# Kernel tuning notes

Measured on AMD Instinct MI355X. Metric: run time of the kernel, lower is better.

Reference implementation:

```python
import jax, jax.numpy as jnp
import numpy as np

NUM_LAYERS = 2
FEATURES = 128
INPUT_SIZE = 128
HIDDEN = 512
BATCH = 128
SEQ_LEN = 512
PRED_LEN = 128


def _uniform(key, shape, fan):
    bound = 1.0 / np.sqrt(fan)
    return jax.random.uniform(key, shape, jnp.float32, -bound, bound)


def setup_inputs() -> dict:
    key = jax.random.key(0)
    ks = jax.random.split(key, 14)
    inp = {}
    inp["x"] = jax.random.normal(ks[0], (BATCH, SEQ_LEN, FEATURES), jnp.float32)
    # encoder Linear(features -> input_size)
    inp["enc_w"] = _uniform(ks[1], (INPUT_SIZE, FEATURES), FEATURES)
    inp["enc_b"] = _uniform(ks[2], (INPUT_SIZE,), FEATURES)
    # decoder Linear(hidden -> input_size)
    inp["dec_w"] = _uniform(ks[3], (INPUT_SIZE, HIDDEN), HIDDEN)
    inp["dec_b"] = _uniform(ks[4], (INPUT_SIZE,), HIDDEN)
    # LSTM layer 0 (input_size -> hidden), gate order i,f,g,o as in PyTorch
    inp["wih0"] = _uniform(ks[5], (4 * HIDDEN, INPUT_SIZE), HIDDEN)
    inp["whh0"] = _uniform(ks[6], (4 * HIDDEN, HIDDEN), HIDDEN)
    inp["bih0"] = _uniform(ks[7], (4 * HIDDEN,), HIDDEN)
    inp["bhh0"] = _uniform(ks[8], (4 * HIDDEN,), HIDDEN)
    # LSTM layer 1 (hidden -> hidden)
    inp["wih1"] = _uniform(ks[9], (4 * HIDDEN, HIDDEN), HIDDEN)
    inp["whh1"] = _uniform(ks[10], (4 * HIDDEN, HIDDEN), HIDDEN)
    inp["bih1"] = _uniform(ks[11], (4 * HIDDEN,), HIDDEN)
    inp["bhh1"] = _uniform(ks[12], (4 * HIDDEN,), HIDDEN)
    inp["pred_len"] = PRED_LEN
    return inp


def _lstm_cell(h, c, inp, wih, whh, bih, bhh):
    g = inp @ wih.T + bih + h @ whh.T + bhh  # [B, 4H]
    i, f, gg, o = jnp.split(g, 4, axis=-1)
    c = jax.nn.sigmoid(f) * c + jax.nn.sigmoid(i) * jnp.tanh(gg)
    h = jax.nn.sigmoid(o) * jnp.tanh(c)
    return h, c


def reference(x, enc_w, enc_b, dec_w, dec_b, wih0, whh0, bih0, bhh0,
              wih1, whh1, bih1, bhh1, pred_len):
    B, S, Fdim = x.shape
    T = S + pred_len - 1
    # pad x to T steps; beyond S the input comes from the previous output
    x_pad = jnp.concatenate([x, jnp.zeros((B, pred_len - 1, Fdim), x.dtype)], axis=1)
    x_t = jnp.transpose(x_pad, (1, 0, 2))  # [T, B, F]

    def step(carry, xs):
        h0, c0, h1, c1, prev_out = carry
        xt, t = xs
        inp = jnp.where(t < S, xt, prev_out)
        e = inp @ enc_w.T + enc_b                    # encoder
        h0, c0 = _lstm_cell(h0, c0, e, wih0, whh0, bih0, bhh0)
        h1, c1 = _lstm_cell(h1, c1, h0, wih1, whh1, bih1, bhh1)
        out = h1 @ dec_w.T + dec_b                   # decoder
        return (h0, c0, h1, c1, out), out

    z = jnp.zeros((B, HIDDEN), x.dtype)
    init = (z, z, z, z, jnp.zeros((B, Fdim), x.dtype))
    _, outs = jax.lax.scan(step, init, (x_t, jnp.arange(T)))
    # keep steps idx >= S-1 (pred_len outputs), back to [B, pred_len, input_size]
    return jnp.transpose(outs[S - 1:], (1, 0, 2))
```

## Files before the change

### kernel.cpp

```cpp
#include <hip/hip_runtime.h>
#include <math.h>

#define HID 512
#define FEAT 128
#define SEQL 512
#define PREDL 128
#define NWG 256
#define HK 516
#define EK 132

typedef float v2f __attribute__((ext_vector_type(2)));

__device__ __forceinline__ float sigf_(float x) { return 1.0f / (1.0f + __expf(-x)); }
__device__ __forceinline__ float tanh_(float x) {
  float ax = fabsf(x);
  float e2 = __expf(-2.0f * ax);
  return copysignf((1.0f - e2) / (1.0f + e2), x);
}
__device__ __forceinline__ v2f mkv2(float a, float b) { v2f r; r[0] = a; r[1] = b; return r; }

__device__ __forceinline__ void stg_sc(float* p, float v) {
  __hip_atomic_store(p, v, __ATOMIC_RELAXED, __HIP_MEMORY_SCOPE_AGENT);
}

__device__ __forceinline__ void bar_arrive(int* __restrict__ bar, int grp,
                                           int phase, int sub, int tid,
                                           bool& last) {
  __syncthreads();
  if (tid == 0) {
    last = false;
    const int a = __hip_atomic_fetch_add(bar + (grp * 8 + sub) * 32, 1,
                                         __ATOMIC_RELAXED, __HIP_MEMORY_SCOPE_AGENT);
    if (a == 4 * phase - 1) {
      const int rr = __hip_atomic_fetch_add(bar + 2048 + grp * 32, 1,
                                            __ATOMIC_RELAXED, __HIP_MEMORY_SCOPE_AGENT);
      if (rr == 8 * phase - 1) {
#pragma unroll
        for (int r = 0; r < 8; ++r)
          __hip_atomic_store(bar + 2304 + (grp * 8 + r) * 32, phase,
                             __ATOMIC_RELAXED, __HIP_MEMORY_SCOPE_AGENT);
        last = true;
      }
    }
  }
  asm volatile("" ::: "memory");
}
__device__ __forceinline__ void bar_wait(int* __restrict__ bar, int grp,
                                         int phase, int rep, int tid,
                                         bool last) {
  asm volatile("" ::: "memory");
  if (tid == 0 && !last) {
    while (__hip_atomic_load(bar + 2304 + (grp * 8 + rep) * 32,
                             __ATOMIC_RELAXED, __HIP_MEMORY_SCOPE_AGENT) < phase)
      __builtin_amdgcn_s_sleep(1);
  }
  __syncthreads();
}

__device__ __forceinline__ void scat(float* __restrict__ dst, int idx, float4 v) {
  const int k = idx >> 2, bq = (idx & 3) * 4;
  dst[(bq + 0) * HK + k] = v.x;
  dst[(bq + 1) * HK + k] = v.y;
  dst[(bq + 2) * HK + k] = v.z;
  dst[(bq + 3) * HK + k] = v.w;
}

__device__ __forceinline__ void stage_hd(float* __restrict__ dst,
                                         const float* __restrict__ blk,
                                         int lane512) {
  const float4* s4 = (const float4*)blk + lane512;
  float4 r0, r1, r2, r3;
  asm volatile(
      "global_load_dwordx4 %0, %4, off sc0 sc1\n\t"
      "global_load_dwordx4 %1, %5, off sc0 sc1\n\t"
      "global_load_dwordx4 %2, %6, off sc0 sc1\n\t"
      "global_load_dwordx4 %3, %7, off sc0 sc1\n\t"
      "s_waitcnt vmcnt(0)"
      : "=&v"(r0), "=&v"(r1), "=&v"(r2), "=&v"(r3)
      : "v"(s4), "v"(s4 + 512), "v"(s4 + 1024), "v"(s4 + 1536)
      : "memory");
  scat(dst, lane512, r0);
  scat(dst, lane512 + 512, r1);
  scat(dst, lane512 + 1024, r2);
  scat(dst, lane512 + 1536, r3);
}

__device__ __forceinline__ void stage_xx(float* __restrict__ dst,
                                         const float* __restrict__ x, int t,
                                         int b0, int lane512) {
  const int bb = lane512 >> 5;
  const int fq = (lane512 & 31) * 4;
  const float4 v =
      *(const float4*)(x + ((size_t)(b0 + bb) * SEQL + t) * FEAT + fq);
  *(float4*)(dst + bb * EK + fq) = v;
}

__device__ __forceinline__ void pkf(v2f& a01, v2f& a23, float4 w, float h) {
  v2f hh; hh[0] = h; hh[1] = h;
  v2f lo; lo[0] = w.x; lo[1] = w.y;
  v2f hi; hi[0] = w.z; hi[1] = w.w;
  a01 = __builtin_elementwise_fma(lo, hh, a01);
  a23 = __builtin_elementwise_fma(hi, hh, a23);
}
__device__ __forceinline__ void gemv_fused8(v2f& a01, v2f& a23,
                                            const float4* __restrict__ W8,
                                            size_t base,
                                            const float* __restrict__ rA,
                                            const float* __restrict__ rB,
                                            int k4b, int k4e) {
#pragma unroll 2
  for (int k4 = k4b; k4 < k4e; ++k4) {
    const float4 hA = *(const float4*)(rA + k4 * 4);
    const float4 hB = *(const float4*)(rB + k4 * 4);
    const size_t o = base + (size_t)k4 * 8;
    pkf(a01, a23, W8[o + 0], hA.x); pkf(a01, a23, W8[o + 1], hB.x);
    pkf(a01, a23, W8[o + 2], hA.y); pkf(a01, a23, W8[o + 3], hB.y);
    pkf(a01, a23, W8[o + 4], hA.z); pkf(a01, a23, W8[o + 5], hB.z);
    pkf(a01, a23, W8[o + 6], hA.w); pkf(a01, a23, W8[o + 7], hB.w);
  }
}
__device__ __forceinline__ void gemv_p4(v2f& a01, v2f& a23,
                                        const float4* __restrict__ W4,
                                        size_t base,
                                        const float* __restrict__ row,
                                        int k4b, int k4e) {
#pragma unroll 4
  for (int k4 = k4b; k4 < k4e; ++k4) {
    const float4 h = *(const float4*)(row + k4 * 4);
    const size_t o = base + (size_t)k4 * 4;
    pkf(a01, a23, W4[o + 0], h.x);
    pkf(a01, a23, W4[o + 1], h.y);
    pkf(a01, a23, W4[o + 2], h.z);
    pkf(a01, a23, W4[o + 3], h.w);
  }
}

__device__ __forceinline__ void act_store(v2f a01, v2f a23, float& c_reg,
                                          float* __restrict__ blk, int cit) {
  const float ig = sigf_(a01[0]), fg = sigf_(a01[1]);
  const float gg = tanh_(a23[0]), og = sigf_(a23[1]);
  const float cn = fg * c_reg + ig * gg;
  c_reg = cn;
  stg_sc(blk + cit, og * tanh_(cn));
}

__global__ __launch_bounds__(1024, 1) void k_teacher(
    const float* __restrict__ x,
    const float* __restrict__ enc2, const float* __restrict__ enc_b,
    const float* __restrict__ wih04, const float* __restrict__ whh04,
    const float* __restrict__ Wf8,
    const float* __restrict__ bih0, const float* __restrict__ bhh0,
    const float* __restrict__ bih1, const float* __restrict__ bhh1,
    float* __restrict__ h0A, float* __restrict__ h0B,
    float* __restrict__ h1A, float* __restrict__ h1B,
    float* __restrict__ cbuf, int* __restrict__ bar) {
  __shared__ float s_h0[16 * HK];
  __shared__ float s_h1[16 * HK];
  __shared__ float s_x[16 * EK];
  __shared__ float s_e[16 * EK];
  __shared__ float4 s_red4[512];

  const int wg = blockIdx.x;
  const int tid = threadIdx.x;
  const int ut = (wg & 7) * 4 + ((wg >> 3) & 3);
  const int bt = wg >> 5;
  const int b0 = bt * 16;
  const int rep = wg & 7;
  const int o = tid & 255;
  const int u = o >> 4, b = o & 15;
  const int ug = ut * 16 + u;
  const int cit = ug * 16 + b;
  const int crewB = tid >> 9;
  const int khalf = (tid >> 8) & 1;
  const int lane512 = tid & 511;

  float* h0b[2] = {h0A, h0B};
  float* h1b[2] = {h1A, h1B};
  const float* sh0row = s_h0 + b * HK;
  const float* sh1row = s_h1 + b * HK;
  const float* serow = s_e + b * EK;

  const float4* W4h = (const float4*)whh04;
  const float4* W4i = (const float4*)wih04;
  const float4* W8f = (const float4*)Wf8;
  const size_t baseH = (size_t)ug * 512;
  const size_t baseI = (size_t)ug * 128;
  const size_t baseF = (size_t)ug * 1024;

  const float bt00 = bih0[ug] + bhh0[ug];
  const float bt01 = bih0[512 + ug] + bhh0[512 + ug];
  const float bt02 = bih0[1024 + ug] + bhh0[1024 + ug];
  const float bt03 = bih0[1536 + ug] + bhh0[1536 + ug];
  const float b10 = bih1[ug] + bhh1[ug];
  const float b11 = bih1[512 + ug] + bhh1[512 + ug];
  const float b12 = bih1[1024 + ug] + bhh1[1024 + ug];
  const float b13 = bih1[1536 + ug] + bhh1[1536 + ug];

  const int eb = tid & 15;
  const int f2 = tid >> 4;
  const float4* EF4 = (const float4*)enc2 + (size_t)f2 * 64;
  const float encb0 = enc_b[f2 * 2], encb1 = enc_b[f2 * 2 + 1];
  const float* sxrow = s_x + eb * EK;

  float c_reg = 0.0f;
  int ph = 0;
  bool lastf = false;

  if (tid < 512) stage_xx(s_x, x, 0, b0, lane512);
  __syncthreads();

  for (int t = 0; t < SEQL; ++t) {
    const float* blk = ((tid < 512) ? h0b[(t + 1) & 1] : h1b[t & 1]) + bt * 8192;
    float* dst = (tid < 512) ? s_h0 : s_h1;
    stage_hd(dst, blk, lane512);

    {
      v2f acc = mkv2(encb0, encb1);
#pragma unroll 8
      for (int k2 = 0; k2 < 64; ++k2) {
        const float4 w = EF4[k2];
        const float hv0 = sxrow[2 * k2], hv1 = sxrow[2 * k2 + 1];
        acc = __builtin_elementwise_fma(mkv2(w.x, w.y), mkv2(hv0, hv0), acc);
        acc = __builtin_elementwise_fma(mkv2(w.z, w.w), mkv2(hv1, hv1), acc);
      }
      s_e[eb * EK + f2 * 2] = acc[0];
      s_e[eb * EK + f2 * 2 + 1] = acc[1];
    }
    __syncthreads();

    v2f a01, a23;
    if (!crewB) {
      if (!khalf) {
        a01 = mkv2(bt00, bt01); a23 = mkv2(bt02, bt03);
        gemv_p4(a01, a23, W4h, baseH, sh0row, 0, 80);
      } else {
        a01 = mkv2(0.f, 0.f); a23 = mkv2(0.f, 0.f);
        gemv_p4(a01, a23, W4h, baseH, sh0row, 80, 128);
        gemv_p4(a01, a23, W4i, baseI, serow, 0, 32);
        s_red4[o] = make_float4(a01[0], a01[1], a23[0], a23[1]);
      }
    } else {
      if (!khalf) {
        a01 = mkv2(b10, b11); a23 = mkv2(b12, b13);
        gemv_fused8(a01, a23, W8f, baseF, sh0row, sh1row, 0, 64);
      } else {
        a01 = mkv2(0.f, 0.f); a23 = mkv2(0.f, 0.f);
        gemv_fused8(a01, a23, W8f, baseF, sh0row, sh1row, 64, 128);
        s_red4[256 + o] = make_float4(a01[0], a01[1], a23[0], a23[1]);
      }
    }
    __syncthreads();
    if (!khalf) {
      const float4 p = s_red4[(crewB ? 256 : 0) + o];
      a01[0] += p.x; a01[1] += p.y; a23[0] += p.z; a23[1] += p.w;
      if (!crewB) act_store(a01, a23, c_reg, h0b[t & 1] + bt * 8192, cit);
      else if (t > 0) act_store(a01, a23, c_reg, h1b[(t + 1) & 1] + bt * 8192, cit);
    }
    bar_arrive(bar, bt, ++ph, rep, tid, lastf);
    if (tid < 512 && t + 1 < SEQL) stage_xx(s_x, x, t + 1, b0, lane512);
    bar_wait(bar, bt, ph, rep, tid, lastf);
  }

  if (tid < 256) cbuf[(size_t)wg * 256 + o] = c_reg;
  else if (tid >= 512 && tid < 768) cbuf[65536 + (size_t)wg * 256 + o] = c_reg;
}

__global__ __launch_bounds__(1024, 1) void k_ar(
    const float* __restrict__ Wa8, const float* __restrict__ Wf8,
    const float* __restrict__ bih0, const float* __restrict__ bhh0,
    const float* __restrict__ bih1, const float* __restrict__ bhh1,
    const float* __restrict__ dec4, const float* __restrict__ dec_b,
    const float* __restrict__ bcomp,
    float* __restrict__ h0A, float* __restrict__ h0B,
    float* __restrict__ h1A, float* __restrict__ h1B,
    float* __restrict__ cbuf, int* __restrict__ bar,
    float* __restrict__ out) {
  __shared__ float s_h0[16 * HK];
  __shared__ float s_h1[16 * HK];
  __shared__ float4 s_red4[768];

  const int wg = blockIdx.x;
  const int tid = threadIdx.x;
  const int ut = (wg & 7) * 4 + ((wg >> 3) & 3);
  const int bt = wg >> 5;
  const int b0 = bt * 16;
  const int rep = wg & 7;
  const int o = tid & 255;
  const int u = o >> 4, b = o & 15;
  const int ug = ut * 16 + u;
  const int cit = ug * 16 + b;
  const int crewB = tid >> 9;
  const int khalf = (tid >> 8) & 1;
  const int lane512 = tid & 511;
  const int q4 = ((tid >> 8) + 2) & 3;

  float* h0b[2] = {h0A, h0B};
  float* h1b[2] = {h1A, h1B};
  const float* sh0row = s_h0 + b * HK;
  const float* sh1row = s_h1 + b * HK;

  const float4* W8a = (const float4*)Wa8;
  const float4* W8f = (const float4*)Wf8;
  const size_t baseG = (size_t)ug * 1024;

  const float ba00 = bih0[ug] + bhh0[ug] + bcomp[ug];
  const float ba01 = bih0[512 + ug] + bhh0[512 + ug] + bcomp[512 + ug];
  const float ba02 = bih0[1024 + ug] + bhh0[1024 + ug] + bcomp[1024 + ug];
  const float ba03 = bih0[1536 + ug] + bhh0[1536 + ug] + bcomp[1536 + ug];
  const float b10 = bih1[ug] + bhh1[ug];
  const float b11 = bih1[512 + ug] + bhh1[512 + ug];
  const float b12 = bih1[1024 + ug] + bhh1[1024 + ug];
  const float b13 = bih1[1536 + ug] + bhh1[1536 + ug];

  const int cb = tid & 511;
  const int jq = cb >> 4, db = cb & 15;
  const float4* D4 = (const float4*)dec4;
  const size_t baseD = (size_t)jq * 512;
  const float db0 = dec_b[jq * 4], db1 = dec_b[jq * 4 + 1];
  const float db2 = dec_b[jq * 4 + 2], db3 = dec_b[jq * 4 + 3];
  const float* dhrow = s_h1 + db * HK;

  float c_reg = 0.0f;
  if (tid < 256) c_reg = cbuf[(size_t)wg * 256 + o];
  else if (tid >= 512 && tid < 768) c_reg = cbuf[65536 + (size_t)wg * 256 + o];

  int ph = 0;
  bool lastf = false;

  if (tid < 512) stage_hd(s_h0, h0b[1] + bt * 8192, lane512);
  else stage_hd(s_h1, h1b[0] + bt * 8192, lane512);
  __syncthreads();
  {
    v2f a01, a23;
    if (q4 == 0) { a01 = mkv2(b10, b11); a23 = mkv2(b12, b13); }
    else { a01 = mkv2(0.f, 0.f); a23 = mkv2(0.f, 0.f); }
    gemv_fused8(a01, a23, W8f, baseG, sh0row, sh1row, q4 * 32, q4 * 32 + 32);
    if (q4) s_red4[(q4 - 1) * 256 + o] = make_float4(a01[0], a01[1], a23[0], a23[1]);
    __syncthreads();
    if (q4 == 0) {
      const float4 p0 = s_red4[o], p1 = s_red4[256 + o], p2 = s_red4[512 + o];
      a01[0] += p0.x + p1.x + p2.x; a01[1] += p0.y + p1.y + p2.y;
      a23[0] += p0.z + p1.z + p2.z; a23[1] += p0.w + p1.w + p2.w;
      act_store(a01, a23, c_reg, h1b[1] + bt * 8192, cit);
    }
  }
  bar_arrive(bar, bt, ++ph, rep, tid, lastf);
  bar_wait(bar, bt, ph, rep, tid, lastf);

  for (int t = SEQL; t < SEQL + PREDL - 1; ++t) {
    if (tid < 512) stage_hd(s_h1, h1b[(t + 1) & 1] + bt * 8192, lane512);
    else stage_hd(s_h0, h0b[(t + 1) & 1] + bt * 8192, lane512);
    __syncthreads();
    v2f a01, a23;
    if (!crewB) {
      if (!khalf) { a01 = mkv2(ba00, ba01); a23 = mkv2(ba02, ba03); }
      else { a01 = mkv2(0.f, 0.f); a23 = mkv2(0.f, 0.f); }
      gemv_fused8(a01, a23, W8a, baseG, sh1row, sh0row,
                  khalf ? 64 : 0, khalf ? 128 : 64);
      if (khalf) s_red4[o] = make_float4(a01[0], a01[1], a23[0], a23[1]);
    } else {
      v2f d01 = mkv2(db0, db1), d23 = mkv2(db2, db3);
      gemv_p4(d01, d23, D4, baseD, dhrow, 0, 128);
      *(float4*)(out + ((size_t)(b0 + db) * PREDL + (t - SEQL)) * FEAT + jq * 4) =
          make_float4(d01[0], d01[1], d23[0], d23[1]);
    }
    __syncthreads();
    if (!crewB && !khalf) {
      const float4 p = s_red4[o];
      a01[0] += p.x; a01[1] += p.y; a23[0] += p.z; a23[1] += p.w;
      act_store(a01, a23, c_reg, h0b[t & 1] + bt * 8192, cit);
    }
    bar_arrive(bar, bt, ++ph, rep, tid, lastf);
    bar_wait(bar, bt, ph, rep, tid, lastf);

    if (tid < 512) stage_hd(s_h0, h0b[t & 1] + bt * 8192, lane512);
    __syncthreads();
    {
      v2f c01, c23;
      if (q4 == 0) { c01 = mkv2(b10, b11); c23 = mkv2(b12, b13); }
      else { c01 = mkv2(0.f, 0.f); c23 = mkv2(0.f, 0.f); }
      gemv_fused8(c01, c23, W8f, baseG, sh0row, sh1row, q4 * 32, q4 * 32 + 32);
      if (q4) s_red4[(q4 - 1) * 256 + o] = make_float4(c01[0], c01[1], c23[0], c23[1]);
      __syncthreads();
      if (q4 == 0) {
        const float4 p0 = s_red4[o], p1 = s_red4[256 + o], p2 = s_red4[512 + o];
        c01[0] += p0.x + p1.x + p2.x; c01[1] += p0.y + p1.y + p2.y;
        c23[0] += p0.z + p1.z + p2.z; c23[1] += p0.w + p1.w + p2.w;
        act_store(c01, c23, c_reg, h1b[t & 1] + bt * 8192, cit);
      }
    }
    bar_arrive(bar, bt, ++ph, rep, tid, lastf);
    bar_wait(bar, bt, ph, rep, tid, lastf);
  }

  if (tid < 512) stage_hd(s_h1, h1b[0] + bt * 8192, lane512);
  __syncthreads();
  if (crewB) {
    v2f d01 = mkv2(db0, db1), d23 = mkv2(db2, db3);
    gemv_p4(d01, d23, D4, baseD, dhrow, 0, 128);
    *(float4*)(out + ((size_t)(b0 + db) * PREDL + (PREDL - 1)) * FEAT + jq * 4) =
        make_float4(d01[0], d01[1], d23[0], d23[1]);
  }
}

__global__ void k_b1(const float* __restrict__ enc_w,
                     const float* __restrict__ dec_w, float* __restrict__ B1) {
  const int idx = blockIdx.x * 256 + threadIdx.x;
  const int j = idx >> 9, m = idx & 511;
  float acc = 0.0f;
  for (int k = 0; k < FEAT; ++k) acc += enc_w[j * FEAT + k] * dec_w[k * HID + m];
  B1[idx] = acc;
}
__global__ void k_te(const float* __restrict__ enc_w,
                     const float* __restrict__ enc_b,
                     const float* __restrict__ dec_b, float* __restrict__ te) {
  const int j = threadIdx.x;
  float acc = enc_b[j];
  for (int k = 0; k < FEAT; ++k) acc += dec_b[k] * enc_w[j * FEAT + k];
  te[j] = acc;
}
__global__ void k_bcomp(const float* __restrict__ wih0,
                        const float* __restrict__ te, float* __restrict__ bc) {
  const int n = blockIdx.x * 256 + threadIdx.x;
  float acc = 0.0f;
  for (int j = 0; j < FEAT; ++j) acc += wih0[n * FEAT + j] * te[j];
  bc[n] = acc;
}
__global__ void k_wa8(const float* __restrict__ wih0,
                      const float* __restrict__ B1,
                      const float* __restrict__ whh0, float* __restrict__ W) {
  const int idx = blockIdx.x * 256 + threadIdx.x;
  const int uu = idx >> 9, k = idx & 511;
  float c[4];
#pragma unroll
  for (int g = 0; g < 4; ++g) {
    const float* wr = wih0 + ((size_t)(g * 512 + uu)) * FEAT;
    float acc = 0.0f;
    for (int j = 0; j < FEAT; ++j) acc += wr[j] * B1[j * HID + k];
    c[g] = acc;
  }
  float4* op = (float4*)(W + ((size_t)(uu * 512 + k)) * 8);
  op[0] = make_float4(c[0], c[1], c[2], c[3]);
  op[1] = make_float4(whh0[((size_t)uu) * 512 + k],
                      whh0[((size_t)(512 + uu)) * 512 + k],
                      whh0[((size_t)(1024 + uu)) * 512 + k],
                      whh0[((size_t)(1536 + uu)) * 512 + k]);
}
__global__ void k_wf8(const float* __restrict__ wih1,
                      const float* __restrict__ whh1, float* __restrict__ W) {
  const int idx = blockIdx.x * 256 + threadIdx.x;
  const int uu = idx >> 9, k = idx & 511;
  float4* op = (float4*)(W + ((size_t)(uu * 512 + k)) * 8);
  op[0] = make_float4(wih1[((size_t)uu) * 512 + k],
                      wih1[((size_t)(512 + uu)) * 512 + k],
                      wih1[((size_t)(1024 + uu)) * 512 + k],
                      wih1[((size_t)(1536 + uu)) * 512 + k]);
  op[1] = make_float4(whh1[((size_t)uu) * 512 + k],
                      whh1[((size_t)(512 + uu)) * 512 + k],
                      whh1[((size_t)(1024 + uu)) * 512 + k],
                      whh1[((size_t)(1536 + uu)) * 512 + k]);
}
__global__ void k_wih04(const float* __restrict__ wih0, float* __restrict__ W) {
  const int idx = blockIdx.x * 256 + threadIdx.x;
  const int uu = idx >> 7, k = idx & 127;
  float4* op = (float4*)(W + ((size_t)idx) * 4);
  op[0] = make_float4(wih0[((size_t)uu) * FEAT + k],
                      wih0[((size_t)(512 + uu)) * FEAT + k],
                      wih0[((size_t)(1024 + uu)) * FEAT + k],
                      wih0[((size_t)(1536 + uu)) * FEAT + k]);
}
__global__ void k_whh04(const float* __restrict__ whh0, float* __restrict__ W) {
  const int idx = blockIdx.x * 256 + threadIdx.x;
  const int uu = idx >> 9, k = idx & 511;
  float4* op = (float4*)(W + ((size_t)idx) * 4);
  op[0] = make_float4(whh0[((size_t)uu) * 512 + k],
                      whh0[((size_t)(512 + uu)) * 512 + k],
                      whh0[((size_t)(1024 + uu)) * 512 + k],
                      whh0[((size_t)(1536 + uu)) * 512 + k]);
}
__global__ void k_enc2(const float* __restrict__ enc_w, float* __restrict__ W) {
  const int idx = blockIdx.x * 256 + threadIdx.x;
  const int f2 = idx >> 7, k = idx & 127;
  W[(size_t)idx * 2 + 0] = enc_w[((size_t)(f2 * 2 + 0)) * FEAT + k];
  W[(size_t)idx * 2 + 1] = enc_w[((size_t)(f2 * 2 + 1)) * FEAT + k];
}
__global__ void k_dec4(const float* __restrict__ dec_w, float* __restrict__ W) {
  const int idx = blockIdx.x * 256 + threadIdx.x;
  const int jq = idx >> 9, k = idx & 511;
  float4* op = (float4*)(W + ((size_t)idx) * 4);
  op[0] = make_float4(dec_w[((size_t)(jq * 4 + 0)) * HID + k],
                      dec_w[((size_t)(jq * 4 + 1)) * HID + k],
                      dec_w[((size_t)(jq * 4 + 2)) * HID + k],
                      dec_w[((size_t)(jq * 4 + 3)) * HID + k]);
}

#define WS_H0A 0
#define WS_H0B 65536
#define WS_H1A 131072
#define WS_H1B 196608
#define WS_CBUF 262144
#define WS_BART 393216
#define WS_BARA 401408
#define WS_B1 409600
#define WS_TE 475136
#define WS_BCOMP 475264
#define WS_WIH04 477312
#define WS_WHH04 739456
#define WS_ENC2 1788032
#define WS_DEC4 1804416
#define WS_WA8 2066560
#define WS_WF8 4163712

extern "C" void kernel_launch(void* const* d_in, const int* in_sizes, int n_in,
                              void* d_out, int out_size, void* d_ws,
                              size_t ws_size, hipStream_t stream) {
  const float* x     = (const float*)d_in[0];
  const float* enc_w = (const float*)d_in[1];
  const float* enc_b = (const float*)d_in[2];
  const float* dec_w = (const float*)d_in[3];
  const float* dec_b = (const float*)d_in[4];
  const float* wih0  = (const float*)d_in[5];
  const float* whh0  = (const float*)d_in[6];
  const float* bih0  = (const float*)d_in[7];
  const float* bhh0  = (const float*)d_in[8];
  const float* wih1  = (const float*)d_in[9];
  const float* whh1  = (const float*)d_in[10];
  const float* bih1  = (const float*)d_in[11];
  const float* bhh1  = (const float*)d_in[12];
  float* out = (float*)d_out;

  float* ws = (float*)d_ws;
  float* h0A = ws + WS_H0A;
  float* h0B = ws + WS_H0B;
  float* h1A = ws + WS_H1A;
  float* h1B = ws + WS_H1B;
  float* cbuf = ws + WS_CBUF;
  int* barT = (int*)(ws + WS_BART);
  int* barA = (int*)(ws + WS_BARA);
  float* B1 = ws + WS_B1;
  float* te = ws + WS_TE;
  float* bcomp = ws + WS_BCOMP;
  float* wih04 = ws + WS_WIH04;
  float* whh04 = ws + WS_WHH04;
  float* enc2 = ws + WS_ENC2;
  float* dec4 = ws + WS_DEC4;
  float* Wa8 = ws + WS_WA8;
  float* Wf8 = ws + WS_WF8;

  (void)hipMemsetAsync(ws, 0, (size_t)262144 * sizeof(float), stream);
  (void)hipMemsetAsync(ws + WS_BART, 0, (size_t)16384 * sizeof(float), stream);

  k_b1<<<256, 256, 0, stream>>>(enc_w, dec_w, B1);
  k_te<<<1, 128, 0, stream>>>(enc_w, enc_b, dec_b, te);
  k_bcomp<<<8, 256, 0, stream>>>(wih0, te, bcomp);
  k_wa8<<<1024, 256, 0, stream>>>(wih0, B1, whh0, Wa8);
  k_wf8<<<1024, 256, 0, stream>>>(wih1, whh1, Wf8);
  k_wih04<<<256, 256, 0, stream>>>(wih0, wih04);
  k_whh04<<<1024, 256, 0, stream>>>(whh0, whh04);
  k_enc2<<<32, 256, 0, stream>>>(enc_w, enc2);
  k_dec4<<<64, 256, 0, stream>>>(dec_w, dec4);

  k_teacher<<<NWG, 1024, 0, stream>>>(
      x, enc2, enc_b, wih04, whh04, Wf8, bih0, bhh0, bih1, bhh1,
      h0A, h0B, h1A, h1B, cbuf, barT);

  k_ar<<<NWG, 1024, 0, stream>>>(
      Wa8, Wf8, bih0, bhh0, bih1, bhh1, dec4, dec_b, bcomp,
      h0A, h0B, h1A, h1B, cbuf, barA, out);
}
```

Baseline: 40.34 ms.

## Replace counter-tree grid barrier with per-workgroup phase flags polled by ballot

Replaces the two-level atomic counter barrier with a flat scheme: each workgroup stores its phase into its own slot, and one wavefront polls all 32 slots in parallel using a ballot. The other waves spin on an LDS phase flag with busy FMA work rather than sleeping. This aims to cut the serialized atomic round trips and wake-up latency on every recurrent step. In exchange it adds more polling traffic and busy-waiting, and it relies on the barrier buffer being zeroed in the new layout.

```diff
diff --git a/kernel.cpp b/kernel.cpp
--- a/kernel.cpp
+++ b/kernel.cpp
@@ -23,36 +23,38 @@
   __hip_atomic_store(p, v, __ATOMIC_RELAXED, __HIP_MEMORY_SCOPE_AGENT);
 }
 
-__device__ __forceinline__ void bar_arrive(int* __restrict__ bar, int grp,
-                                           int phase, int sub, int tid,
-                                           bool& last) {
+__device__ __forceinline__ void bar_arrive2(int* __restrict__ bar, int grp,
+                                            int idx, int phase, int tid) {
   __syncthreads();
-  if (tid == 0) {
-    last = false;
-    const int a = __hip_atomic_fetch_add(bar + (grp * 8 + sub) * 32, 1,
-                                         __ATOMIC_RELAXED, __HIP_MEMORY_SCOPE_AGENT);
-    if (a == 4 * phase - 1) {
-      const int rr = __hip_atomic_fetch_add(bar + 2048 + grp * 32, 1,
-                                            __ATOMIC_RELAXED, __HIP_MEMORY_SCOPE_AGENT);
-      if (rr == 8 * phase - 1) {
+  if (tid == 0)
+    __hip_atomic_store(bar + grp * 32 + idx, phase, __ATOMIC_RELAXED,
+                       __HIP_MEMORY_SCOPE_AGENT);
+  asm volatile("" ::: "memory");
+}
+__device__ __forceinline__ void bar_wait2(int* __restrict__ bar, int grp,
+                                          int phase, int tid,
+                                          int* __restrict__ ldsph) {
+  asm volatile("" ::: "memory");
+  if (tid < 64) {
+    int done = 0;
+    while (!done) {
+      int v = phase;
+      if (tid < 32)
+        v = __hip_atomic_load(bar + grp * 32 + tid, __ATOMIC_RELAXED,
+                              __HIP_MEMORY_SCOPE_AGENT);
+      done = (__ballot(v >= phase) == 0xFFFFFFFFFFFFFFFFULL);
+    }
+    if (tid == 0)
+      __hip_atomic_store(ldsph, phase, __ATOMIC_RELAXED,
+                         __HIP_MEMORY_SCOPE_WORKGROUP);
+  } else {
+    float z = 1.0f;
+    while (__hip_atomic_load(ldsph, __ATOMIC_RELAXED,
+                             __HIP_MEMORY_SCOPE_WORKGROUP) < phase) {
 #pragma unroll
-        for (int r = 0; r < 8; ++r)
-          __hip_atomic_store(bar + 2304 + (grp * 8 + r) * 32, phase,
-                             __ATOMIC_RELAXED, __HIP_MEMORY_SCOPE_AGENT);
-        last = true;
-      }
-    }
-  }
-  asm volatile("" ::: "memory");
-}
-__device__ __forceinline__ void bar_wait(int* __restrict__ bar, int grp,
-                                         int phase, int rep, int tid,
-                                         bool last) {
-  asm volatile("" ::: "memory");
-  if (tid == 0 && !last) {
-    while (__hip_atomic_load(bar + 2304 + (grp * 8 + rep) * 32,
-                             __ATOMIC_RELAXED, __HIP_MEMORY_SCOPE_AGENT) < phase)
-      __builtin_amdgcn_s_sleep(1);
+      for (int i = 0; i < 64; ++i) z = __builtin_fmaf(z, 1.0000001f, 1.0e-9f);
+      asm volatile("" : "+v"(z));
+    }
   }
   __syncthreads();
 }
@@ -159,13 +161,14 @@
   __shared__ float s_x[16 * EK];
   __shared__ float s_e[16 * EK];
   __shared__ float4 s_red4[512];
+  __shared__ int lds_ph;
 
   const int wg = blockIdx.x;
   const int tid = threadIdx.x;
   const int ut = (wg & 7) * 4 + ((wg >> 3) & 3);
   const int bt = wg >> 5;
   const int b0 = bt * 16;
-  const int rep = wg & 7;
+  const int idx32 = wg & 31;
   const int o = tid & 255;
   const int u = o >> 4, b = o & 15;
   const int ug = ut * 16 + u;
@@ -204,8 +207,8 @@
 
   float c_reg = 0.0f;
   int ph = 0;
-  bool lastf = false;
-
+
+  if (tid == 0) lds_ph = 0;
   if (tid < 512) stage_xx(s_x, x, 0, b0, lane512);
   __syncthreads();
 
@@ -256,9 +259,9 @@
       if (!crewB) act_store(a01, a23, c_reg, h0b[t & 1] + bt * 8192, cit);
       else if (t > 0) act_store(a01, a23, c_reg, h1b[(t + 1) & 1] + bt * 8192, cit);
     }
-    bar_arrive(bar, bt, ++ph, rep, tid, lastf);
+    bar_arrive2(bar, bt, idx32, ++ph, tid);
     if (tid < 512 && t + 1 < SEQL) stage_xx(s_x, x, t + 1, b0, lane512);
-    bar_wait(bar, bt, ph, rep, tid, lastf);
+    bar_wait2(bar, bt, ph, tid, &lds_ph);
   }
 
   if (tid < 256) cbuf[(size_t)wg * 256 + o] = c_reg;
@@ -278,13 +281,14 @@
   __shared__ float s_h0[16 * HK];
   __shared__ float s_h1[16 * HK];
   __shared__ float4 s_red4[768];
+  __shared__ int lds_ph;
 
   const int wg = blockIdx.x;
   const int tid = threadIdx.x;
   const int ut = (wg & 7) * 4 + ((wg >> 3) & 3);
   const int bt = wg >> 5;
   const int b0 = bt * 16;
-  const int rep = wg & 7;
+  const int idx32 = wg & 31;
   const int o = tid & 255;
   const int u = o >> 4, b = o & 15;
   const int ug = ut * 16 + u;
@@ -325,7 +329,7 @@
   else if (tid >= 512 && tid < 768) c_reg = cbuf[65536 + (size_t)wg * 256 + o];
 
   int ph = 0;
-  bool lastf = false;
+  if (tid == 0) lds_ph = 0;
 
   if (tid < 512) stage_hd(s_h0, h0b[1] + bt * 8192, lane512);
   else stage_hd(s_h1, h1b[0] + bt * 8192, lane512);
@@ -344,8 +348,8 @@
       act_store(a01, a23, c_reg, h1b[1] + bt * 8192, cit);
     }
   }
-  bar_arrive(bar, bt, ++ph, rep, tid, lastf);
-  bar_wait(bar, bt, ph, rep, tid, lastf);
+  bar_arrive2(bar, bt, idx32, ++ph, tid);
+  bar_wait2(bar, bt, ph, tid, &lds_ph);
 
   for (int t = SEQL; t < SEQL + PREDL - 1; ++t) {
     if (tid < 512) stage_hd(s_h1, h1b[(t + 1) & 1] + bt * 8192, lane512);
@@ -370,8 +374,8 @@
       a01[0] += p.x; a01[1] += p.y; a23[0] += p.z; a23[1] += p.w;
       act_store(a01, a23, c_reg, h0b[t & 1] + bt * 8192, cit);
     }
-    bar_arrive(bar, bt, ++ph, rep, tid, lastf);
-    bar_wait(bar, bt, ph, rep, tid, lastf);
+    bar_arrive2(bar, bt, idx32, ++ph, tid);
+    bar_wait2(bar, bt, ph, tid, &lds_ph);
 
     if (tid < 512) stage_hd(s_h0, h0b[t & 1] + bt * 8192, lane512);
     __syncthreads();
@@ -389,8 +393,8 @@
         act_store(c01, c23, c_reg, h1b[t & 1] + bt * 8192, cit);
       }
     }
-    bar_arrive(bar, bt, ++ph, rep, tid, lastf);
-    bar_wait(bar, bt, ph, rep, tid, lastf);
+    bar_arrive2(bar, bt, idx32, ++ph, tid);
+    bar_wait2(bar, bt, ph, tid, &lds_ph);
   }
 
   if (tid < 512) stage_hd(s_h1, h1b[0] + bt * 8192, lane512);
```

Measured after the change: 40.79 ms. About the same (+1.1%).
